# Optimization experiments

Measured on AMD Instinct MI355X. Metric: run time of the kernel, lower is better.

## Reference

```python
import jax, jax.numpy as jnp
import numpy as np

K = 3
DILATION = 1
DG = 1  # deformable groups


def _deform_conv2d(x, offsets, mask, weight, bias, k=K, dilation=DILATION, dg=DG):
    # x: [B, C, H, W]; offsets: [B, dg*2*k*k, H, W]; mask: [B, dg*k*k, H, W]
    # weight: [O, C, k, k]; bias: [O]
    B, C, H, W = x.shape
    O = weight.shape[0]
    Cg = C // dg
    kk = k * k
    pad = (k // 2) * dilation

    # base sampling grid per kernel tap (stride=1)
    ky, kx = jnp.meshgrid(jnp.arange(k), jnp.arange(k), indexing='ij')
    ky = ky.reshape(kk)
    kx = kx.reshape(kk)
    base_y = (jnp.arange(H)[None, :, None] - pad + ky[:, None, None] * dilation)  # [kk,H,1]
    base_x = (jnp.arange(W)[None, None, :] - pad + kx[:, None, None] * dilation)  # [kk,1,W]

    off = offsets.reshape(B, dg, kk, 2, H, W)
    py = base_y[None, None].astype(x.dtype) + off[:, :, :, 0]  # [B,dg,kk,H,W]
    px = base_x[None, None].astype(x.dtype) + off[:, :, :, 1]  # [B,dg,kk,H,W]

    y0 = jnp.floor(py)
    x0 = jnp.floor(px)
    wy1 = py - y0  # frac weights
    wx1 = px - x0
    wy0 = 1.0 - wy1
    wx0 = 1.0 - wx1

    img = x.reshape(B, dg, Cg, H * W)

    def gather(yi, xi):
        # yi, xi: float integer-valued coords [B,dg,kk,H,W]; zero outside bounds
        valid = (yi >= 0) & (yi <= H - 1) & (xi >= 0) & (xi <= W - 1)
        yc = jnp.clip(yi, 0, H - 1).astype(jnp.int32)
        xc = jnp.clip(xi, 0, W - 1).astype(jnp.int32)
        idx = (yc * W + xc).reshape(B, dg, 1, kk * H * W)
        vals = jnp.take_along_axis(img, idx, axis=3).reshape(B, dg, Cg, kk, H, W)
        return vals * valid.reshape(B, dg, 1, kk, H, W).astype(x.dtype)

    def w5(a):  # lift [B,dg,kk,H,W] -> [B,dg,1,kk,H,W]
        return a.reshape(B, dg, 1, kk, H, W)

    sampled = (gather(y0, x0) * w5(wy0 * wx0)
               + gather(y0, x0 + 1) * w5(wy0 * wx1)
               + gather(y0 + 1, x0) * w5(wy1 * wx0)
               + gather(y0 + 1, x0 + 1) * w5(wy1 * wx1))  # [B,dg,Cg,kk,H,W]

    sampled = sampled * mask.reshape(B, dg, 1, kk, H, W)
    sampled = sampled.reshape(B, C, kk, H, W)

    out = jnp.einsum('bckhw,ock->bohw', sampled, weight.reshape(O, C, kk))
    return out + bias[None, :, None, None]


def setup_inputs() -> dict:
    key = jax.random.key(0)
    k1, k2, k3, k4, k5 = jax.random.split(key, 5)
    B, C, O, H, W = 8, 128, 128, 64, 64
    x = jax.random.normal(k1, (B, C, H, W), dtype=jnp.float32)
    offsets = jax.random.normal(k2, (B, DG * 2 * K * K, H, W), dtype=jnp.float32)
    mask = jax.random.uniform(k3, (B, DG * K * K, H, W), dtype=jnp.float32)
    fan_in = C * K * K
    weight = jax.random.normal(k4, (O, C, K, K), dtype=jnp.float32) / np.sqrt(fan_in)
    bias = jax.random.normal(k5, (O,), dtype=jnp.float32) * 0.01
    return {"x": x, "offsets": offsets, "mask": mask, "weight": weight, "bias": bias}


def reference(x, offsets, mask, weight, bias):
    return _deform_conv2d(x, offsets, mask, weight, bias)
```

## Files before the change

kernel.cpp:

```cpp
#include <hip/hip_runtime.h>
#include <math.h>

constexpr int Bn = 8, Cn = 128, On = 128, Hn = 64, Wn = 64;
constexpr int KK = 9, PAD = 1, BDIM = 256;
constexpr int PXB = 32;
constexpr int CG = 16;
constexpr int NG = Cn / CG;
constexpr int KG = 160;
constexpr int KTOT = NG * KG;
constexpr int BANDH = 10;
constexpr int XSTP = 660;
constexpr int ASTW = 88;
constexpr int ME = KK * PXB;

typedef __attribute__((ext_vector_type(8))) short bf16x8;
typedef __attribute__((ext_vector_type(4))) float f32x4;
typedef unsigned short u16;
typedef unsigned int u32;

__device__ inline u16 f2bf(float f) {
    union { float f; u32 u; } v; v.f = f;
    return (u16)((v.u + 0x7FFFu + ((v.u >> 16) & 1u)) >> 16);
}
__device__ inline u32 pk2bf(float a, float b) {
    return (u32)f2bf(a) | ((u32)f2bf(b) << 16);
}
__device__ inline float bflo(u32 w) { return __uint_as_float(w << 16); }
__device__ inline float bfhi(u32 w) { return __uint_as_float(w & 0xFFFF0000u); }

__global__ void wprep_kernel(const float* __restrict__ w, u16* __restrict__ wbf) {
    const int e = blockIdx.x * BDIM + threadIdx.x;
    const int o  = e / KTOT;
    const int kp = e - o * KTOT;
    const int g  = kp / KG;
    const int r  = kp - g * KG;
    const int t  = r >> 4;
    const int cl = r & 15;
    float v = 0.f;
    if (t < KK) v = w[o * (Cn * KK) + (g * CG + cl) * KK + t];
    wbf[e] = f2bf(v);
}

__global__ __launch_bounds__(BDIM, 2)
void dcn_mfma_kernel(const float* __restrict__ x,
                     const float* __restrict__ offs,
                     const float* __restrict__ mask,
                     const u16*   __restrict__ wbf,
                     const float* __restrict__ bias,
                     float* __restrict__ out)
{
    __shared__ __align__(16) u32 pband[8 * XSTP];
    __shared__ __align__(16) u32 ashw[PXB * ASTW];

    const int tid    = threadIdx.x;
    const int b      = blockIdx.x & 7;
    const int rem    = blockIdx.x >> 3;
    const int h      = rem >> 1;
    const int pxbase = (rem & 1) * PXB;
    const int r0     = min(max(h - 4, 0), Hn - BANDH);

    const int s_px4  = tid & 15;
    const int s_pair = (tid >> 4) & 7;
    float4 bnda[5], bndb[5];
    {
        #pragma unroll
        for (int it = 0; it < 5; ++it) {
            const int row = (tid + it * BDIM) >> 7;
            const float* base = x + (((size_t)(b * Cn + 2 * s_pair)) << 12)
                                + (r0 + row) * Wn + (s_px4 << 2);
            bnda[it] = *(const float4*)base;
            bndb[it] = *(const float4*)(base + 4096);
        }
    }

    float4 mw[2]; int2 mq[2]; int2 mi[2];
    #pragma unroll
    for (int it = 0; it < 2; ++it) {
        mw[it] = make_float4(0.f, 0.f, 0.f, 0.f);
        mq[it] = make_int2(0, 0);
        mi[it] = make_int2(7, 7);
        const int e = tid + it * BDIM;
        if (e < ME) {
            const int t = e >> 5, px = e & 31, pg = pxbase + px;
            const int ty = t / 3, tx = t - ty * 3;
            const float oy = offs[((b * 18 + 2 * t    ) * Hn + h) * Wn + pg];
            const float ox = offs[((b * 18 + 2 * t + 1) * Hn + h) * Wn + pg];
            const float m  = mask[((b * KK + t) * Hn + h) * Wn + pg];
            const float py = (float)(h - PAD + ty) + oy;
            const float qx = (float)(pg - PAD + tx) + ox;
            const float fy = floorf(py), fx = floorf(qx);
            const float wy1 = py - fy, wx1 = qx - fx;
            const float wy0 = 1.f - wy1, wx0 = 1.f - wx1;
            const int y0 = (int)fy, x0 = (int)fx;
            const bool cx0 = (x0 >= 0) && (x0 < Wn);
            const bool cx1 = (x0 >= -1) && (x0 < Wn - 1);
            const float wr[2] = { wy0, wy1 };
            float wout[4]; int qout[2], iout[2];
            #pragma unroll
            for (int j = 0; j < 2; ++j) {
                const int yr = y0 + j;
                const bool rv = (yr >= 0) && (yr < Hn);
                wout[2 * j]     = (rv && cx0) ? wr[j] * wx0 * m : 0.f;
                wout[2 * j + 1] = (rv && cx1) ? wr[j] * wx1 * m : 0.f;
                int qv;
                if (!rv || (!cx0 && !cx1)) qv = r0 << 8;
                else                       qv = (yr << 8) | (x0 + 1);
                const int row = qv >> 8;
                const bool inband = (row >= r0) && (row < r0 + BANDH);
                qout[j] = inband ? qv : ~qv;
                const int rl = min(max(row - r0, 0), BANDH - 1);
                iout[j] = (rl << 6) + (qv & 255) + 7;
            }
            mw[it] = make_float4(wout[0], wout[1], wout[2], wout[3]);
            mq[it] = make_int2(qout[0], qout[1]);
            mi[it] = make_int2(iout[0], iout[1]);
        }
    }

    {
        #pragma unroll
        for (int it = 0; it < 5; ++it) {
            const int row = (tid + it * BDIM) >> 7;
            u32* d = &pband[s_pair * XSTP + row * 64 + 8 + (s_px4 << 2)];
            *(uint4*)d = make_uint4(pk2bf(bnda[it].x, bndb[it].x),
                                    pk2bf(bnda[it].y, bndb[it].y),
                                    pk2bf(bnda[it].z, bndb[it].z),
                                    pk2bf(bnda[it].w, bndb[it].w));
        }
        if (tid < 128) {
            const int pr = tid >> 4, ws = tid & 15;
            pband[pr * XSTP + (ws < 8 ? ws : 640 + ws)] = 0;
        }
        ashw[(tid >> 3) * ASTW + 72 + (tid & 7)] = 0;
    }
    __syncthreads();

    const int wv = tid >> 6, ln = tid & 63, quad = ln >> 4, l16 = ln & 15;
    const u16* wrow0 = wbf + (size_t)(wv * 32 + l16) * KTOT;

    f32x4 acc[2][2];
    #pragma unroll
    for (int mt = 0; mt < 2; ++mt)
        #pragma unroll
        for (int nt = 0; nt < 2; ++nt) acc[mt][nt] = (f32x4){0.f, 0.f, 0.f, 0.f};

    for (int g = 0; g < NG; ++g) {
        #pragma unroll
        for (int it = 0; it < 2; ++it) {
            const int e = tid + it * BDIM;
            if (e < ME) {
                const int t = e >> 5, px = e & 31;
                const float4 w  = mw[it];
                const int2   q  = mq[it];
                const int2   ix = mi[it];
                u32 ct0[8], ct1[8], cb0[8], cb1[8];
                #pragma unroll
                for (int c2 = 0; c2 < 8; ++c2) {
                    const u32* pc = &pband[c2 * XSTP];
                    ct0[c2] = pc[ix.x]; ct1[c2] = pc[ix.x + 1];
                    cb0[c2] = pc[ix.y]; cb1[c2] = pc[ix.y + 1];
                }
                if (q.x < 0) {
                    const int qv = ~q.x, yr = qv >> 8, xx = (qv & 255) - 1;
                    const int a0 = max(xx, 0), a1 = min(xx + 1, Wn - 1);
                    const float* gp = x + (((size_t)(b * Cn + g * CG)) << 12) + yr * Wn;
                    #pragma unroll
                    for (int c2 = 0; c2 < 8; ++c2) {
                        const float* g0 = gp + ((2 * c2) << 12);
                        ct0[c2] = pk2bf(g0[a0], g0[4096 + a0]);
                        ct1[c2] = pk2bf(g0[a1], g0[4096 + a1]);
                    }
                }
                if (q.y < 0) {
                    const int qv = ~q.y, yr = qv >> 8, xx = (qv & 255) - 1;
                    const int a0 = max(xx, 0), a1 = min(xx + 1, Wn - 1);
                    const float* gp = x + (((size_t)(b * Cn + g * CG)) << 12) + yr * Wn;
                    #pragma unroll
                    for (int c2 = 0; c2 < 8; ++c2) {
                        const float* g0 = gp + ((2 * c2) << 12);
                        cb0[c2] = pk2bf(g0[a0], g0[4096 + a0]);
                        cb1[c2] = pk2bf(g0[a1], g0[4096 + a1]);
                    }
                }
                u32 avp[8];
                #pragma unroll
                for (int c2 = 0; c2 < 8; ++c2) {
                    const float va = fmaf(w.x, bflo(ct0[c2]), fmaf(w.y, bflo(ct1[c2]),
                                     fmaf(w.z, bflo(cb0[c2]), w.w * bflo(cb1[c2]))));
                    const float vb = fmaf(w.x, bfhi(ct0[c2]), fmaf(w.y, bfhi(ct1[c2]),
                                     fmaf(w.z, bfhi(cb0[c2]), w.w * bfhi(cb1[c2]))));
                    avp[c2] = pk2bf(va, vb);
                }
                u32* d = &ashw[px * ASTW + (t << 3)];
                *(uint4*)d       = make_uint4(avp[0], avp[1], avp[2], avp[3]);
                *(uint4*)(d + 4) = make_uint4(avp[4], avp[5], avp[6], avp[7]);
            }
        }
        __syncthreads();

        if (g + 1 < NG) {
            #pragma unroll
            for (int it = 0; it < 5; ++it) {
                const int row = (tid + it * BDIM) >> 7;
                const float* base = x + (((size_t)(b * Cn + (g + 1) * CG + 2 * s_pair)) << 12)
                                    + (r0 + row) * Wn + (s_px4 << 2);
                bnda[it] = *(const float4*)base;
                bndb[it] = *(const float4*)(base + 4096);
            }
        }

        #pragma unroll
        for (int s = 0; s < 5; ++s) {
            const int kg = g * KG + s * 32 + quad * 8;
            const int kd = s * 16 + quad * 4;
            const bf16x8 a0 = *(const bf16x8*)(wrow0 + kg);
            const bf16x8 a1 = *(const bf16x8*)(wrow0 + 16 * KTOT + kg);
            union BF { uint4 u; bf16x8 v; } b0, b1;
            b0.u = *(const uint4*)&ashw[(0 * 16 + l16) * ASTW + kd];
            b1.u = *(const uint4*)&ashw[(1 * 16 + l16) * ASTW + kd];
            acc[0][0] = __builtin_amdgcn_mfma_f32_16x16x32_bf16(a0, b0.v, acc[0][0], 0, 0, 0);
            acc[0][1] = __builtin_amdgcn_mfma_f32_16x16x32_bf16(a0, b1.v, acc[0][1], 0, 0, 0);
            acc[1][0] = __builtin_amdgcn_mfma_f32_16x16x32_bf16(a1, b0.v, acc[1][0], 0, 0, 0);
            acc[1][1] = __builtin_amdgcn_mfma_f32_16x16x32_bf16(a1, b1.v, acc[1][1], 0, 0, 0);
        }

        if (g + 1 < NG) {
            #pragma unroll
            for (int it = 0; it < 5; ++it) {
                const int row = (tid + it * BDIM) >> 7;
                u32* d = &pband[s_pair * XSTP + row * 64 + 8 + (s_px4 << 2)];
                *(uint4*)d = make_uint4(pk2bf(bnda[it].x, bndb[it].x),
                                        pk2bf(bnda[it].y, bndb[it].y),
                                        pk2bf(bnda[it].z, bndb[it].z),
                                        pk2bf(bnda[it].w, bndb[it].w));
            }
        }
        __syncthreads();
    }

    float* tr = (float*)pband;
    #pragma unroll
    for (int mt = 0; mt < 2; ++mt)
        #pragma unroll
        for (int nt = 0; nt < 2; ++nt)
            #pragma unroll
            for (int r = 0; r < 4; ++r) {
                const int o  = wv * 32 + mt * 16 + quad * 4 + r;
                const int px = nt * 16 + l16;
                tr[o * 36 + px] = acc[mt][nt][r] + bias[o];
            }
    __syncthreads();
    float* ob = out + (size_t)b * On * Hn * Wn + h * Wn + pxbase;
    {
        const int orow = tid >> 3, ck = tid & 7;
        #pragma unroll
        for (int it = 0; it < 4; ++it) {
            const int o = it * 32 + orow;
            const float4 v = *(const float4*)&tr[o * 36 + (ck << 2)];
            *(float4*)&ob[(size_t)o * (Hn * Wn) + (ck << 2)] = v;
        }
    }
}

constexpr int FB_PXB = 32, FB_CCH = 4, FB_NCT = FB_CCH * KK, FB_MW = KK * FB_PXB;

#define FMA4(A, S, W)                          \
    A.x = fmaf((S).x, (W), A.x);               \
    A.y = fmaf((S).y, (W), A.y);               \
    A.z = fmaf((S).z, (W), A.z);               \
    A.w = fmaf((S).w, (W), A.w);

__global__ __launch_bounds__(BDIM, 4)
void dcn_fb_kernel(const float* __restrict__ x,
                   const float* __restrict__ offs,
                   const float* __restrict__ mask,
                   const float* __restrict__ weight,
                   const float* __restrict__ bias,
                   float* __restrict__ out)
{
    __shared__ float wmeta[4 * FB_MW];
    __shared__ int   imeta[4 * FB_MW];
    __shared__ float ssh[FB_NCT * FB_PXB];
    __shared__ float wsh[FB_NCT * On];

    const int tid    = threadIdx.x;
    const int b      = blockIdx.x & 7;
    const int rem    = blockIdx.x >> 3;
    const int h      = rem >> 1;
    const int pxbase = (rem & 1) * FB_PXB;

    for (int e = tid; e < FB_MW; e += BDIM) {
        const int t  = e >> 5;
        const int px = e & 31;
        const int pg = pxbase + px;
        const int ty = t / 3, tx = t - ty * 3;
        const float oy = offs[((b * 18 + 2 * t    ) * Hn + h) * Wn + pg];
        const float ox = offs[((b * 18 + 2 * t + 1) * Hn + h) * Wn + pg];
        const float m  = mask[((b * KK + t) * Hn + h) * Wn + pg];
        const float py = (float)(h - PAD + ty) + oy;
        const float qx = (float)(pg - PAD + tx) + ox;
        const float y0 = floorf(py), x0 = floorf(qx);
        const float wy1 = py - y0, wx1 = qx - x0;
        const float wy0 = 1.f - wy1, wx0 = 1.f - wx1;
        const float cw[4] = { wy0 * wx0, wy0 * wx1, wy1 * wx0, wy1 * wx1 };
        #pragma unroll
        for (int k = 0; k < 4; ++k) {
            const float yk = y0 + (float)(k >> 1);
            const float xk = x0 + (float)(k & 1);
            const bool valid = (yk >= 0.f) && (yk <= (float)(Hn - 1)) &&
                               (xk >= 0.f) && (xk <= (float)(Wn - 1));
            const int yc = (int)fminf(fmaxf(yk, 0.f), (float)(Hn - 1));
            const int xc = (int)fminf(fmaxf(xk, 0.f), (float)(Wn - 1));
            wmeta[k * FB_MW + e] = valid ? cw[k] * m : 0.f;
            imeta[k * FB_MW + e] = yc * Wn + xc;
        }
    }
    __syncthreads();

    const int px0 = (tid & 7) << 2;
    const int oo  = (tid >> 3) << 2;

    float4 acc[4];
    #pragma unroll
    for (int j = 0; j < 4; ++j) acc[j] = make_float4(0.f, 0.f, 0.f, 0.f);

    for (int cb = 0; cb < Cn / FB_CCH; ++cb) {
        #pragma unroll
        for (int it = 0; it < (FB_NCT * On) / BDIM; ++it) {
            const int e = tid + it * BDIM;
            const int r = e >> 7;
            const int o = e & 127;
            wsh[r * On + o] = weight[o * (Cn * KK) + cb * FB_NCT + r];
        }
        for (int e = tid; e < FB_NCT * FB_PXB; e += BDIM) {
            const int px = e & 31;
            const int ct = e >> 5;
            const int c  = ct / 9;
            const int mb = (ct - c * 9) * FB_PXB + px;
            const float* xp = x + (((b * Cn) + cb * FB_CCH + c) << 12);
            float v =  wmeta[mb]              * xp[imeta[mb]];
            v = fmaf(wmeta[FB_MW     + mb], xp[imeta[FB_MW     + mb]], v);
            v = fmaf(wmeta[2 * FB_MW + mb], xp[imeta[2 * FB_MW + mb]], v);
            v = fmaf(wmeta[3 * FB_MW + mb], xp[imeta[3 * FB_MW + mb]], v);
            ssh[ct * FB_PXB + px] = v;
        }
        __syncthreads();

        #pragma unroll 6
        for (int ct = 0; ct < FB_NCT; ++ct) {
            const float4 sv = *(const float4*)&ssh[ct * FB_PXB + px0];
            const float4 wa = *(const float4*)&wsh[ct * On + oo];
            FMA4(acc[0], sv, wa.x);
            FMA4(acc[1], sv, wa.y);
            FMA4(acc[2], sv, wa.z);
            FMA4(acc[3], sv, wa.w);
        }
        __syncthreads();
    }

    #pragma unroll
    for (int j = 0; j < 4; ++j) {
        const float bv = bias[oo + j];
        float4 r = acc[j];
        r.x += bv; r.y += bv; r.z += bv; r.w += bv;
        *(float4*)&out[((b * On + oo + j) * Hn + h) * Wn + pxbase + px0] = r;
    }
}

extern "C" void kernel_launch(void* const* d_in, const int* in_sizes, int n_in,
                              void* d_out, int out_size, void* d_ws, size_t ws_size,
                              hipStream_t stream) {
    const float* x      = (const float*)d_in[0];
    const float* offs   = (const float*)d_in[1];
    const float* mask   = (const float*)d_in[2];
    const float* weight = (const float*)d_in[3];
    const float* bias   = (const float*)d_in[4];
    float* out = (float*)d_out;

    const size_t need = (size_t)On * KTOT * sizeof(u16);
    if (d_ws != nullptr && ws_size >= need) {
        u16* wbf = (u16*)d_ws;
        wprep_kernel<<<dim3(On * KTOT / BDIM), dim3(BDIM), 0, stream>>>(weight, wbf);
        dcn_mfma_kernel<<<dim3(Bn * Hn * 2), dim3(BDIM), 0, stream>>>(
            x, offs, mask, wbf, bias, out);
    } else {
        dcn_fb_kernel<<<dim3(Bn * Hn * 2), dim3(BDIM), 0, stream>>>(
            x, offs, mask, weight, bias, out);
    }
}
```

Baseline: 154.5 us.

## Halve LDS band to 8-channel stages to raise occupancy to six blocks

Each 16-channel group is split into two 8-channel stages. The LDS band buffer shrinks to 4 channel-pairs, the per-thread prefetch registers drop from 5 to 3 float4 pairs, and launch bounds rise from 2 to 6 blocks per SM so more blocks can be resident to hide gather latency. MFMA still runs once per 16 channels, after the second stage has filled the other half of the A tile. In exchange the number of block-wide barriers doubles and the register budget per thread gets much tighter, which risks spills.

```diff
diff --git a/kernel.cpp b/kernel.cpp
--- a/kernel.cpp
+++ b/kernel.cpp
@@ -4,14 +4,14 @@
 constexpr int Bn = 8, Cn = 128, On = 128, Hn = 64, Wn = 64;
 constexpr int KK = 9, PAD = 1, BDIM = 256;
 constexpr int PXB = 32;
-constexpr int CG = 16;
-constexpr int NG = Cn / CG;
+constexpr int NST = 16;
 constexpr int KG = 160;
-constexpr int KTOT = NG * KG;
+constexpr int KTOT = 8 * KG;
 constexpr int BANDH = 10;
 constexpr int XSTP = 660;
 constexpr int ASTW = 88;
 constexpr int ME = KK * PXB;
+constexpr int SMEMW = 4 * XSTP + PXB * ASTW;
 
 typedef __attribute__((ext_vector_type(8))) short bf16x8;
 typedef __attribute__((ext_vector_type(4))) float f32x4;
@@ -37,11 +37,11 @@
     const int t  = r >> 4;
     const int cl = r & 15;
     float v = 0.f;
-    if (t < KK) v = w[o * (Cn * KK) + (g * CG + cl) * KK + t];
+    if (t < KK) v = w[o * (Cn * KK) + (g * 16 + cl) * KK + t];
     wbf[e] = f2bf(v);
 }
 
-__global__ __launch_bounds__(BDIM, 2)
+__global__ __launch_bounds__(BDIM, 6)
 void dcn_mfma_kernel(const float* __restrict__ x,
                      const float* __restrict__ offs,
                      const float* __restrict__ mask,
@@ -49,8 +49,9 @@
                      const float* __restrict__ bias,
                      float* __restrict__ out)
 {
-    __shared__ __align__(16) u32 pband[8 * XSTP];
-    __shared__ __align__(16) u32 ashw[PXB * ASTW];
+    __shared__ __align__(16) u32 smem[SMEMW];
+    u32* const pband = smem;
+    u32* const ashw  = smem + 4 * XSTP;
 
     const int tid    = threadIdx.x;
     const int b      = blockIdx.x & 7;
@@ -60,16 +61,19 @@
     const int r0     = min(max(h - 4, 0), Hn - BANDH);
 
     const int s_px4  = tid & 15;
-    const int s_pair = (tid >> 4) & 7;
-    float4 bnda[5], bndb[5];
+    const int s_pair = (tid >> 4) & 3;
+    float4 bnda[3], bndb[3];
     {
         #pragma unroll
-        for (int it = 0; it < 5; ++it) {
-            const int row = (tid + it * BDIM) >> 7;
-            const float* base = x + (((size_t)(b * Cn + 2 * s_pair)) << 12)
-                                + (r0 + row) * Wn + (s_px4 << 2);
-            bnda[it] = *(const float4*)base;
-            bndb[it] = *(const float4*)(base + 4096);
+        for (int it = 0; it < 3; ++it) {
+            const int tau = tid + it * BDIM;
+            if (tau < 640) {
+                const int row = tau >> 6;
+                const float* base = x + (((size_t)(b * Cn + 2 * s_pair)) << 12)
+                                    + (r0 + row) * Wn + (s_px4 << 2);
+                bnda[it] = *(const float4*)base;
+                bndb[it] = *(const float4*)(base + 4096);
+            }
         }
     }
 
@@ -119,17 +123,20 @@
 
     {
         #pragma unroll
-        for (int it = 0; it < 5; ++it) {
-            const int row = (tid + it * BDIM) >> 7;
-            u32* d = &pband[s_pair * XSTP + row * 64 + 8 + (s_px4 << 2)];
-            *(uint4*)d = make_uint4(pk2bf(bnda[it].x, bndb[it].x),
-                                    pk2bf(bnda[it].y, bndb[it].y),
-                                    pk2bf(bnda[it].z, bndb[it].z),
-                                    pk2bf(bnda[it].w, bndb[it].w));
-        }
-        if (tid < 128) {
-            const int pr = tid >> 4, ws = tid & 15;
-            pband[pr * XSTP + (ws < 8 ? ws : 640 + ws)] = 0;
+        for (int it = 0; it < 3; ++it) {
+            const int tau = tid + it * BDIM;
+            if (tau < 640) {
+                const int row = tau >> 6;
+                u32* d = &pband[s_pair * XSTP + row * 64 + 8 + (s_px4 << 2)];
+                *(uint4*)d = make_uint4(pk2bf(bnda[it].x, bndb[it].x),
+                                        pk2bf(bnda[it].y, bndb[it].y),
+                                        pk2bf(bnda[it].z, bndb[it].z),
+                                        pk2bf(bnda[it].w, bndb[it].w));
+            }
+        }
+        if (tid < 80) {
+            const int pr = tid / 20, w = tid % 20;
+            pband[pr * XSTP + (w < 8 ? w : 640 + w)] = 0;
         }
         ashw[(tid >> 3) * ASTW + 72 + (tid & 7)] = 0;
     }
@@ -144,7 +151,10 @@
         #pragma unroll
         for (int nt = 0; nt < 2; ++nt) acc[mt][nt] = (f32x4){0.f, 0.f, 0.f, 0.f};
 
-    for (int g = 0; g < NG; ++g) {
+    for (int sg = 0; sg < NST; ++sg) {
+        const int c0 = sg << 3;
+        const int klo = (sg & 1) << 2;
+
         #pragma unroll
         for (int it = 0; it < 2; ++it) {
             const int e = tid + it * BDIM;
@@ -153,92 +163,103 @@
                 const float4 w  = mw[it];
                 const int2   q  = mq[it];
                 const int2   ix = mi[it];
-                u32 ct0[8], ct1[8], cb0[8], cb1[8];
                 #pragma unroll
-                for (int c2 = 0; c2 < 8; ++c2) {
-                    const u32* pc = &pband[c2 * XSTP];
-                    ct0[c2] = pc[ix.x]; ct1[c2] = pc[ix.x + 1];
-                    cb0[c2] = pc[ix.y]; cb1[c2] = pc[ix.y + 1];
+                for (int hf = 0; hf < 2; ++hf) {
+                    u32 ct0[2], ct1[2], cb0[2], cb1[2];
+                    #pragma unroll
+                    for (int pp = 0; pp < 2; ++pp) {
+                        const u32* pc = &pband[(2 * hf + pp) * XSTP];
+                        ct0[pp] = pc[ix.x]; ct1[pp] = pc[ix.x + 1];
+                        cb0[pp] = pc[ix.y]; cb1[pp] = pc[ix.y + 1];
+                    }
+                    if (q.x < 0) {
+                        const int qv = ~q.x, yr = qv >> 8, xx = (qv & 255) - 1;
+                        const int a0 = max(xx, 0), a1 = min(xx + 1, Wn - 1);
+                        const float* gp = x + (((size_t)(b * Cn + c0)) << 12) + yr * Wn;
+                        #pragma unroll
+                        for (int pp = 0; pp < 2; ++pp) {
+                            const float* g0 = gp + ((2 * (2 * hf + pp)) << 12);
+                            ct0[pp] = pk2bf(g0[a0], g0[4096 + a0]);
+                            ct1[pp] = pk2bf(g0[a1], g0[4096 + a1]);
+                        }
+                    }
+                    if (q.y < 0) {
+                        const int qv = ~q.y, yr = qv >> 8, xx = (qv & 255) - 1;
+                        const int a0 = max(xx, 0), a1 = min(xx + 1, Wn - 1);
+                        const float* gp = x + (((size_t)(b * Cn + c0)) << 12) + yr * Wn;
+                        #pragma unroll
+                        for (int pp = 0; pp < 2; ++pp) {
+                            const float* g0 = gp + ((2 * (2 * hf + pp)) << 12);
+                            cb0[pp] = pk2bf(g0[a0], g0[4096 + a0]);
+                            cb1[pp] = pk2bf(g0[a1], g0[4096 + a1]);
+                        }
+                    }
+                    u32 avp[2];
+                    #pragma unroll
+                    for (int pp = 0; pp < 2; ++pp) {
+                        const float va = fmaf(w.x, bflo(ct0[pp]), fmaf(w.y, bflo(ct1[pp]),
+                                         fmaf(w.z, bflo(cb0[pp]), w.w * bflo(cb1[pp]))));
+                        const float vb = fmaf(w.x, bfhi(ct0[pp]), fmaf(w.y, bfhi(ct1[pp]),
+                                         fmaf(w.z, bfhi(cb0[pp]), w.w * bfhi(cb1[pp]))));
+                        avp[pp] = pk2bf(va, vb);
+                    }
+                    *(uint2*)&ashw[px * ASTW + (t << 3) + klo + 2 * hf] =
+                        make_uint2(avp[0], avp[1]);
                 }
-                if (q.x < 0) {
-                    const int qv = ~q.x, yr = qv >> 8, xx = (qv & 255) - 1;
-                    const int a0 = max(xx, 0), a1 = min(xx + 1, Wn - 1);
-                    const float* gp = x + (((size_t)(b * Cn + g * CG)) << 12) + yr * Wn;
-                    #pragma unroll
-                    for (int c2 = 0; c2 < 8; ++c2) {
-                        const float* g0 = gp + ((2 * c2) << 12);
-                        ct0[c2] = pk2bf(g0[a0], g0[4096 + a0]);
-                        ct1[c2] = pk2bf(g0[a1], g0[4096 + a1]);
-                    }
+            }
+        }
+
+        if (sg + 1 < NST) {
+            #pragma unroll
+            for (int it = 0; it < 3; ++it) {
+                const int tau = tid + it * BDIM;
+                if (tau < 640) {
+                    const int row = tau >> 6;
+                    const float* base = x + (((size_t)(b * Cn + (sg + 1) * 8 + 2 * s_pair)) << 12)
+                                        + (r0 + row) * Wn + (s_px4 << 2);
+                    bnda[it] = *(const float4*)base;
+                    bndb[it] = *(const float4*)(base + 4096);
                 }
-                if (q.y < 0) {
-                    const int qv = ~q.y, yr = qv >> 8, xx = (qv & 255) - 1;
-                    const int a0 = max(xx, 0), a1 = min(xx + 1, Wn - 1);
-                    const float* gp = x + (((size_t)(b * Cn + g * CG)) << 12) + yr * Wn;
-                    #pragma unroll
-                    for (int c2 = 0; c2 < 8; ++c2) {
-                        const float* g0 = gp + ((2 * c2) << 12);
-                        cb0[c2] = pk2bf(g0[a0], g0[4096 + a0]);
-                        cb1[c2] = pk2bf(g0[a1], g0[4096 + a1]);
-                    }
+            }
+        }
+        __syncthreads();
+
+        if (sg & 1) {
+            const int g = sg >> 1;
+            #pragma unroll
+            for (int s = 0; s < 5; ++s) {
+                const int kg = g * KG + s * 32 + quad * 8;
+                const int kd = s * 16 + quad * 4;
+                const bf16x8 a0 = *(const bf16x8*)(wrow0 + kg);
+                const bf16x8 a1 = *(const bf16x8*)(wrow0 + 16 * KTOT + kg);
+                union BF { uint4 u; bf16x8 v; } b0, b1;
+                b0.u = *(const uint4*)&ashw[(0 * 16 + l16) * ASTW + kd];
+                b1.u = *(const uint4*)&ashw[(1 * 16 + l16) * ASTW + kd];
+                acc[0][0] = __builtin_amdgcn_mfma_f32_16x16x32_bf16(a0, b0.v, acc[0][0], 0, 0, 0);
+                acc[0][1] = __builtin_amdgcn_mfma_f32_16x16x32_bf16(a0, b1.v, acc[0][1], 0, 0, 0);
+                acc[1][0] = __builtin_amdgcn_mfma_f32_16x16x32_bf16(a1, b0.v, acc[1][0], 0, 0, 0);
+                acc[1][1] = __builtin_amdgcn_mfma_f32_16x16x32_bf16(a1, b1.v, acc[1][1], 0, 0, 0);
+            }
+        }
+
+        if (sg + 1 < NST) {
+            #pragma unroll
+            for (int it = 0; it < 3; ++it) {
+                const int tau = tid + it * BDIM;
+                if (tau < 640) {
+                    const int row = tau >> 6;
+                    u32* d = &pband[s_pair * XSTP + row * 64 + 8 + (s_px4 << 2)];
+                    *(uint4*)d = make_uint4(pk2bf(bnda[it].x, bndb[it].x),
+                                            pk2bf(bnda[it].y, bndb[it].y),
+                                            pk2bf(bnda[it].z, bndb[it].z),
+                                            pk2bf(bnda[it].w, bndb[it].w));
                 }
-                u32 avp[8];
-                #pragma unroll
-                for (int c2 = 0; c2 < 8; ++c2) {
-                    const float va = fmaf(w.x, bflo(ct0[c2]), fmaf(w.y, bflo(ct1[c2]),
-                                     fmaf(w.z, bflo(cb0[c2]), w.w * bflo(cb1[c2]))));
-                    const float vb = fmaf(w.x, bfhi(ct0[c2]), fmaf(w.y, bfhi(ct1[c2]),
-                                     fmaf(w.z, bfhi(cb0[c2]), w.w * bfhi(cb1[c2]))));
-                    avp[c2] = pk2bf(va, vb);
-                }
-                u32* d = &ashw[px * ASTW + (t << 3)];
-                *(uint4*)d       = make_uint4(avp[0], avp[1], avp[2], avp[3]);
-                *(uint4*)(d + 4) = make_uint4(avp[4], avp[5], avp[6], avp[7]);
             }
         }
         __syncthreads();
-
-        if (g + 1 < NG) {
-            #pragma unroll
-            for (int it = 0; it < 5; ++it) {
-                const int row = (tid + it * BDIM) >> 7;
-                const float* base = x + (((size_t)(b * Cn + (g + 1) * CG + 2 * s_pair)) << 12)
-                                    + (r0 + row) * Wn + (s_px4 << 2);
-                bnda[it] = *(const float4*)base;
-                bndb[it] = *(const float4*)(base + 4096);
-            }
-        }
-
-        #pragma unroll
-        for (int s = 0; s < 5; ++s) {
-            const int kg = g * KG + s * 32 + quad * 8;
-            const int kd = s * 16 + quad * 4;
-            const bf16x8 a0 = *(const bf16x8*)(wrow0 + kg);
-            const bf16x8 a1 = *(const bf16x8*)(wrow0 + 16 * KTOT + kg);
-            union BF { uint4 u; bf16x8 v; } b0, b1;
-            b0.u = *(const uint4*)&ashw[(0 * 16 + l16) * ASTW + kd];
-            b1.u = *(const uint4*)&ashw[(1 * 16 + l16) * ASTW + kd];
-            acc[0][0] = __builtin_amdgcn_mfma_f32_16x16x32_bf16(a0, b0.v, acc[0][0], 0, 0, 0);
-            acc[0][1] = __builtin_amdgcn_mfma_f32_16x16x32_bf16(a0, b1.v, acc[0][1], 0, 0, 0);
-            acc[1][0] = __builtin_amdgcn_mfma_f32_16x16x32_bf16(a1, b0.v, acc[1][0], 0, 0, 0);
-            acc[1][1] = __builtin_amdgcn_mfma_f32_16x16x32_bf16(a1, b1.v, acc[1][1], 0, 0, 0);
-        }
-
-        if (g + 1 < NG) {
-            #pragma unroll
-            for (int it = 0; it < 5; ++it) {
-                const int row = (tid + it * BDIM) >> 7;
-                u32* d = &pband[s_pair * XSTP + row * 64 + 8 + (s_px4 << 2)];
-                *(uint4*)d = make_uint4(pk2bf(bnda[it].x, bndb[it].x),
-                                        pk2bf(bnda[it].y, bndb[it].y),
-                                        pk2bf(bnda[it].z, bndb[it].z),
-                                        pk2bf(bnda[it].w, bndb[it].w));
-            }
-        }
-        __syncthreads();
-    }
-
-    float* tr = (float*)pband;
+    }
+
+    float* tr = (float*)smem;
     #pragma unroll
     for (int mt = 0; mt < 2; ++mt)
         #pragma unroll
```

Result: slower. 264.4 us (+71.1%).
